# Kernel tuning notes

Hardware: AMD Instinct MI355X
Metric: run time of the kernel (lower is better)

Reference implementation:

```python
import jax, jax.numpy as jnp
import numpy as np


def _patch_indices():
    # 36 positions (6x6 grid), each gathering a 3x3 window of 6-channel squares
    # from the flattened 385-vector: index = x*48 + y*6 + c
    idx = []
    for i in range(36):
        x, y = i // 6, i % 6
        rows = []
        for ox in range(3):
            for oy in range(3):
                base = (x + ox) * 48 + (y + oy) * 6
                rows.extend(range(base, base + 6))
        idx.append(rows)
    return jnp.asarray(np.array(idx, dtype=np.int32))  # [36, 54]


_IDX = _patch_indices()


def _crelu(v):
    return jnp.clip(v, -1.0, 1.0)


def setup_inputs() -> dict:
    key = jax.random.key(0)
    ks = jax.random.split(key, 13)
    B = 131072
    inp = jax.random.normal(ks[0], (B, 385), dtype=jnp.float32)
    s = 0.2  # small init scale
    # sight stack: 54 -> 8 -> 8 -> 1  (stored as [in, out])
    W1 = jax.random.normal(ks[1], (54, 8), jnp.float32) * s
    b1 = jax.random.normal(ks[2], (8,), jnp.float32) * s
    W2 = jax.random.normal(ks[3], (8, 8), jnp.float32) * s
    b2 = jax.random.normal(ks[4], (8,), jnp.float32) * s
    W3 = jax.random.normal(ks[5], (8, 1), jnp.float32) * s
    b3 = jax.random.normal(ks[6], (1,), jnp.float32) * s
    # evaluation stack: 37 -> 16 -> 16 -> 1
    E1 = jax.random.normal(ks[7], (37, 16), jnp.float32) * s
    c1 = jax.random.normal(ks[8], (16,), jnp.float32) * s
    E2 = jax.random.normal(ks[9], (16, 16), jnp.float32) * s
    c2 = jax.random.normal(ks[10], (16,), jnp.float32) * s
    E3 = jax.random.normal(ks[11], (16, 1), jnp.float32) * s
    c3 = jax.random.normal(ks[12], (1,), jnp.float32) * s
    return {"inp": inp, "W1": W1, "b1": b1, "W2": W2, "b2": b2,
            "W3": W3, "b3": b3, "E1": E1, "c1": c1, "E2": E2, "c2": c2,
            "E3": E3, "c3": c3}


def reference(inp, W1, b1, W2, b2, W3, b3, E1, c1, E2, c2, E3, c3):
    # inp: [B, 385]
    patches = inp[:, _IDX]                       # [B, 36, 54] windowed gather
    h = _crelu(jnp.einsum('bpf,fo->bpo', patches, W1) + b1)   # [B, 36, 8]
    h = _crelu(jnp.einsum('bpf,fo->bpo', h, W2) + b2)         # [B, 36, 8]
    v = _crelu(jnp.einsum('bpf,fo->bpo', h, W3) + b3)[..., 0]  # [B, 36]
    vision = jnp.concatenate([v, inp[:, 384:385]], axis=1)    # [B, 37]
    g = _crelu(vision @ E1 + c1)                 # [B, 16]
    g = _crelu(g @ E2 + c2)                      # [B, 16]
    out = _crelu(g @ E3 + c3)                    # [B, 1]
    return out
```

## Files before the change

kernel.cpp:

```cpp
#include <hip/hip_runtime.h>

typedef __attribute__((ext_vector_type(8))) short short8;
typedef __attribute__((ext_vector_type(4))) float float4v;

__device__ __forceinline__ float crelu(float v) {
    return fminf(1.0f, fmaxf(-1.0f, v));
}
__device__ __forceinline__ uint f2bf_u(float v) {
    uint u = __float_as_uint(v);
    u += 0x7fffu + ((u >> 16) & 1u);
    return u >> 16;
}
__device__ __forceinline__ ushort f2bf(float v) { return (ushort)f2bf_u(v); }
__device__ __forceinline__ float bf2f_lo(uint u) { return __uint_as_float(u << 16); }
__device__ __forceinline__ float bf2f_hi(uint u) { return __uint_as_float(u & 0xffff0000u); }
__device__ __forceinline__ uint cvt_pk_bf16(float a, float b) {
    uint r;
    asm("v_cvt_pk_bf16_f32 %0, %1, %2" : "=v"(r) : "v"(a), "v"(b));
    return r;
}

#define ROW 385
#define BT  16

#define SLAB_BYTES 6656
#define E1T_OFF 960
#define E2T_OFF 3776
#define E1T_LD  44

__global__ __launch_bounds__(256, 6)
void lila_wave(const float* __restrict__ inp,
               const float* __restrict__ W1, const float* __restrict__ b1,
               const float* __restrict__ W2, const float* __restrict__ b2,
               const float* __restrict__ W3, const float* __restrict__ b3,
               const float* __restrict__ E1, const float* __restrict__ c1,
               const float* __restrict__ E2, const float* __restrict__ c2,
               const float* __restrict__ E3, const float* __restrict__ c3,
               float* __restrict__ out)
{
    __shared__ __align__(16) char slab_all[4 * SLAB_BYTES];

    const int tid  = threadIdx.x;
    const int lane = tid & 63;
    const int wv   = tid >> 6;
    const int quad = lane >> 4;
    const int nn   = lane & 15;
    const int m0   = quad * 8;

    char*   slab  = slab_all + wv * SLAB_BYTES;
    ushort* board = (ushort*)slab;
    ushort* hbuf  = (ushort*)(slab + 4352);
    float*  vis   = (float*)slab;
    float*  g1    = (float*)(slab + 640);
    float*  e1t   = (float*)(slab + E1T_OFF);
    ushort* e2t   = (ushort*)(slab + E2T_OFF);

    const long long b0w = (long long)blockIdx.x * BT + wv * 4;

    short8 bfr[3];
    #pragma unroll
    for (int rr = 0; rr < 3; ++rr) {
        #pragma unroll
        for (int j = 0; j < 8; ++j) {
            int k = m0 + j, oy = k >> 3, c = k & 7;
            float w = (oy < 3 && c < 6 && nn < 8)
                    ? W1[(rr * 18 + oy * 6 + c) * 8 + nn] : 0.0f;
            bfr[rr][j] = (short)f2bf(w);
        }
    }
    const float bias1 = (nn < 8) ? b1[nn] : 0.0f;

    short8 w2fh, w2fl;
    {
        const int colq = nn - quad * 8;
        #pragma unroll
        for (int j = 0; j < 8; ++j) {
            float w = (quad < 2 && colq >= 0 && colq < 8) ? W2[j * 8 + colq] : 0.0f;
            uint hb2 = f2bf_u(w);
            float wr = w - __uint_as_float(hb2 << 16);
            w2fh[j] = (short)hb2;
            w2fl[j] = (short)f2bf(wr);
        }
    }
    const float b2v = b2[nn & 7];
    const float w3v = W3[nn & 7];
    const float b3v = b3[0];
    const float c1v = c1[nn];
    const float c2v = c2[nn];
    const float e3v = E3[nn];

    const int r   = lane >> 4;
    const int c16 = lane & 15;
    const float* gr = inp + (b0w + r) * ROW;

    if (c16 < 4) {
        uint4 z = {0u, 0u, 0u, 0u};
        *(uint4*)(board + r * 544 + 512 + c16 * 8) = z;
    }
    #pragma unroll
    for (int u = 0; u < 4; ++u) {
        int cell = c16 + 16 * u;
        int g = cell * 6;
        float4 q0 = *(const float4*)(gr + g);
        float2 q1 = *(const float2*)(gr + g + 4);
        uint4 pk;
        pk.x = cvt_pk_bf16(q0.x, q0.y);
        pk.y = cvt_pk_bf16(q0.z, q0.w);
        pk.z = cvt_pk_bf16(q1.x, q1.y);
        pk.w = 0u;
        *(uint4*)(board + r * 544 + cell * 8) = pk;
    }
    const float cen = gr[384];

    asm volatile("" ::: "memory");

    {
        const int lb0 = nn >> 2, y0 = nn & 3;
        const ushort* base = board + lb0 * 544 + 8 * y0 + m0;
        union { uint4 u; short8 s; } rw[3];
        rw[0].u = *(const uint4*)(base);
        rw[1].u = *(const uint4*)(base + 64);
        #pragma unroll
        for (int x = 0; x < 6; ++x) {
            rw[(x + 2) % 3].u = *(const uint4*)(base + (x + 2) * 64);
            float4v acc = { bias1, bias1, bias1, bias1 };
            acc = __builtin_amdgcn_mfma_f32_16x16x32_bf16(rw[x % 3].s,       bfr[0], acc, 0, 0, 0);
            acc = __builtin_amdgcn_mfma_f32_16x16x32_bf16(rw[(x + 1) % 3].s, bfr[1], acc, 0, 0, 0);
            acc = __builtin_amdgcn_mfma_f32_16x16x32_bf16(rw[(x + 2) % 3].s, bfr[2], acc, 0, 0, 0);
            if (nn < 8) {
                uint w01 = cvt_pk_bf16(crelu(acc[0]), crelu(acc[1]));
                uint w23 = cvt_pk_bf16(crelu(acc[2]), crelu(acc[3]));
                ushort* hb = hbuf + (quad * 36 + x * 6) * 8 + nn;
                hb[0]  = (ushort)w01;
                hb[8]  = (ushort)(w01 >> 16);
                hb[16] = (ushort)w23;
                hb[24] = (ushort)(w23 >> 16);
            }
        }
    }
    {
        const int lb1 = (nn >> 1) & 3, y1 = 4 + (nn & 1);
        const ushort* base = board + lb1 * 544 + 8 * y1 + m0;
        union { uint4 u; short8 s; } rw[3];
        rw[0].u = *(const uint4*)(base);
        rw[1].u = *(const uint4*)(base + 64);
        #pragma unroll
        for (int x = 0; x < 6; ++x) {
            rw[(x + 2) % 3].u = *(const uint4*)(base + (x + 2) * 64);
            float4v acc = { bias1, bias1, bias1, bias1 };
            acc = __builtin_amdgcn_mfma_f32_16x16x32_bf16(rw[x % 3].s,       bfr[0], acc, 0, 0, 0);
            acc = __builtin_amdgcn_mfma_f32_16x16x32_bf16(rw[(x + 1) % 3].s, bfr[1], acc, 0, 0, 0);
            acc = __builtin_amdgcn_mfma_f32_16x16x32_bf16(rw[(x + 2) % 3].s, bfr[2], acc, 0, 0, 0);
            if (quad < 2 && nn < 8) {
                uint w01 = cvt_pk_bf16(crelu(acc[0]), crelu(acc[1]));
                uint w23 = cvt_pk_bf16(crelu(acc[2]), crelu(acc[3]));
                ushort* hb = hbuf + ((2 * quad) * 36 + x * 6 + 4) * 8 + nn;
                hb[0]   = (ushort)w01;
                hb[8]   = (ushort)(w01 >> 16);
                hb[288] = (ushort)w23;
                hb[296] = (ushort)(w23 >> 16);
            }
        }
    }

    asm volatile("" ::: "memory");

    float e1g[10];
    #pragma unroll
    for (int k = 0; k < 9; ++k) e1g[k] = E1[lane + 64 * k];
    if (lane < 16) e1g[9] = E1[lane + 576];
    float e2g[4];
    #pragma unroll
    for (int k = 0; k < 4; ++k) e2g[k] = E2[lane + 64 * k];

    {
        #pragma unroll
        for (int t = 0; t < 5; ++t) {
            union { uint4 u; short8 s; } av;
            av.u.x = 0u; av.u.y = 0u; av.u.z = 0u; av.u.w = 0u;
            int tsk = t * 16 + nn + (quad ? 80 : 0);
            if (quad < 2 && (t < 4 || quad == 0))
                av.u = *(const uint4*)(hbuf + tsk * 8);
            float4v acc = { b2v, b2v, b2v, b2v };
            acc = __builtin_amdgcn_mfma_f32_16x16x32_bf16(av.s, w2fh, acc, 0, 0, 0);
            acc = __builtin_amdgcn_mfma_f32_16x16x32_bf16(av.s, w2fl, acc, 0, 0, 0);
            float vsum[4];
            #pragma unroll
            for (int i = 0; i < 4; ++i) {
                float vv = crelu(acc[i]) * w3v;
                vv += __shfl_xor(vv, 1);
                vv += __shfl_xor(vv, 2);
                vv += __shfl_xor(vv, 4);
                vsum[i] = vv;
            }
            const bool isA = (nn == 0);
            if ((nn & 7) == 0 && (isA || t < 4)) {
                int task = (isA ? 0 : 80) + t * 16 + quad * 4;
                uint lb = (uint)task / 36u;
                uint p  = (uint)task - 36u * lb;
                float4 o4;
                o4.x = crelu(vsum[0] + b3v);
                o4.y = crelu(vsum[1] + b3v);
                o4.z = crelu(vsum[2] + b3v);
                o4.w = crelu(vsum[3] + b3v);
                *(float4*)(vis + lb * 40 + p) = o4;
            }
        }
    }

    #pragma unroll
    for (int k = 0; k < 9; ++k) e1t[nn * E1T_LD + r + 4 * k] = e1g[k];
    if (lane < 16) e1t[nn * E1T_LD + 36] = e1g[9];
    #pragma unroll
    for (int k = 0; k < 4; ++k) e2t[nn * 16 + r + 4 * k] = f2bf(e2g[k]);

    asm volatile("" ::: "memory");

    {
        const int o = nn;
        float a = c1v;
        #pragma unroll
        for (int fi = 0; fi < 9; ++fi) {
            float4 vv = *(const float4*)(vis + r * 40 + fi * 4);
            float4 ev = *(const float4*)(e1t + o * E1T_LD + fi * 4);
            a = fmaf(vv.x, ev.x, a);
            a = fmaf(vv.y, ev.y, a);
            a = fmaf(vv.z, ev.z, a);
            a = fmaf(vv.w, ev.w, a);
        }
        a = fmaf(cen, e1t[o * E1T_LD + 36], a);
        g1[r * 20 + o] = crelu(a);

        asm volatile("" ::: "memory");

        uint4 e2a = *(const uint4*)(e2t + o * 16);
        uint4 e2b = *(const uint4*)(e2t + o * 16 + 8);
        float a2 = c2v;
        #pragma unroll
        for (int fi = 0; fi < 4; ++fi) {
            float4 gv = *(const float4*)(g1 + r * 20 + fi * 4);
            uint w01 = (fi < 2) ? (fi == 0 ? e2a.x : e2a.z) : (fi == 2 ? e2b.x : e2b.z);
            uint w23 = (fi < 2) ? (fi == 0 ? e2a.y : e2a.w) : (fi == 2 ? e2b.y : e2b.w);
            a2 = fmaf(gv.x, bf2f_lo(w01), a2);
            a2 = fmaf(gv.y, bf2f_hi(w01), a2);
            a2 = fmaf(gv.z, bf2f_lo(w23), a2);
            a2 = fmaf(gv.w, bf2f_hi(w23), a2);
        }
        float tv = crelu(a2) * e3v;
        tv += __shfl_xor(tv, 1);
        tv += __shfl_xor(tv, 2);
        tv += __shfl_xor(tv, 4);
        tv += __shfl_xor(tv, 8);
        if (o == 0) out[b0w + r] = crelu(tv + c3[0]);
    }
}

extern "C" void kernel_launch(void* const* d_in, const int* in_sizes, int n_in,
                              void* d_out, int out_size, void* d_ws, size_t ws_size,
                              hipStream_t stream)
{
    const float* inp = (const float*)d_in[0];
    const float* W1  = (const float*)d_in[1];
    const float* b1  = (const float*)d_in[2];
    const float* W2  = (const float*)d_in[3];
    const float* b2  = (const float*)d_in[4];
    const float* W3  = (const float*)d_in[5];
    const float* b3  = (const float*)d_in[6];
    const float* E1  = (const float*)d_in[7];
    const float* c1  = (const float*)d_in[8];
    const float* E2  = (const float*)d_in[9];
    const float* c2  = (const float*)d_in[10];
    const float* E3  = (const float*)d_in[11];
    const float* c3  = (const float*)d_in[12];
    float* out = (float*)d_out;

    int B = in_sizes[0] / ROW;
    int grid = B / BT;
    lila_wave<<<grid, 256, 0, stream>>>(inp, W1, b1, W2, b2, W3, b3,
                                        E1, c1, E2, c2, E3, c3, out);
}
```

Measured before the change: 295.8 us.

## Make kernel persistent over 8 row groups with register prefetch and shared weight tables

Each wave now processes 8 groups of 4 rows in a loop instead of one, prefetching the next group's input into registers while computing the current one. The weight loads and the E1/E2 transposed tables are moved out of the per-group path: the tables are built once per block by wave 0 in shared memory and published with a barrier. The grid shrinks by a factor of 8 and launch bounds drop to 4 blocks per SIMD, trading occupancy and extra registers for amortized setup and overlap of global loads with compute.

```diff
diff --git a/kernel.cpp b/kernel.cpp
--- a/kernel.cpp
+++ b/kernel.cpp
@@ -22,13 +22,13 @@
 
 #define ROW 385
 #define BT  16
-
-#define SLAB_BYTES 6656
-#define E1T_OFF 960
-#define E2T_OFF 3776
-#define E1T_LD  44
-
-__global__ __launch_bounds__(256, 6)
+#define NG  8
+
+#define TAB_BYTES  3392
+#define SLAB_BYTES 7616
+#define E1T_LD     44
+
+__global__ __launch_bounds__(256, 4)
 void lila_wave(const float* __restrict__ inp,
                const float* __restrict__ W1, const float* __restrict__ b1,
                const float* __restrict__ W2, const float* __restrict__ b2,
@@ -38,7 +38,7 @@
                const float* __restrict__ E3, const float* __restrict__ c3,
                float* __restrict__ out)
 {
-    __shared__ __align__(16) char slab_all[4 * SLAB_BYTES];
+    __shared__ __align__(16) char slab_all[TAB_BYTES + 4 * SLAB_BYTES];
 
     const int tid  = threadIdx.x;
     const int lane = tid & 63;
@@ -46,16 +46,31 @@
     const int quad = lane >> 4;
     const int nn   = lane & 15;
     const int m0   = quad * 8;
-
-    char*   slab  = slab_all + wv * SLAB_BYTES;
+    const int r    = lane >> 4;
+    const int c16  = lane & 15;
+
+    char*   slab  = slab_all + TAB_BYTES + wv * SLAB_BYTES;
     ushort* board = (ushort*)slab;
     ushort* hbuf  = (ushort*)(slab + 4352);
-    float*  vis   = (float*)slab;
-    float*  g1    = (float*)(slab + 640);
-    float*  e1t   = (float*)(slab + E1T_OFF);
-    ushort* e2t   = (ushort*)(slab + E2T_OFF);
-
-    const long long b0w = (long long)blockIdx.x * BT + wv * 4;
+    float*  vis   = (float*)(slab + 6656);
+    float*  g1    = (float*)(slab + 7296);
+    float*  e1t   = (float*)slab_all;
+    ushort* e2t   = (ushort*)(slab_all + 2816);
+
+    const long long s0 = (long long)blockIdx.x * (BT * NG) + (long long)wv * (4 * NG);
+    const float* grp = inp + s0 * ROW;
+
+    float4 p4[4]; float2 p2[4]; float cen_c;
+    {
+        const float* gr = grp + r * ROW;
+        #pragma unroll
+        for (int u = 0; u < 4; ++u) {
+            int g6 = (c16 + 16 * u) * 6;
+            p4[u] = *(const float4*)(gr + g6);
+            p2[u] = *(const float2*)(gr + g6 + 4);
+        }
+        cen_c = gr[384];
+    }
 
     short8 bfr[3];
     #pragma unroll
@@ -89,169 +104,195 @@
     const float c2v = c2[nn];
     const float e3v = E3[nn];
 
-    const int r   = lane >> 4;
-    const int c16 = lane & 15;
-    const float* gr = inp + (b0w + r) * ROW;
+    if (wv == 0) {
+        float e1g[10];
+        #pragma unroll
+        for (int k = 0; k < 9; ++k) e1g[k] = E1[lane + 64 * k];
+        if (lane < 16) e1g[9] = E1[lane + 576];
+        float e2g[4];
+        #pragma unroll
+        for (int k = 0; k < 4; ++k) e2g[k] = E2[lane + 64 * k];
+        #pragma unroll
+        for (int k = 0; k < 9; ++k) e1t[nn * E1T_LD + r + 4 * k] = e1g[k];
+        if (lane < 16) e1t[nn * E1T_LD + 36] = e1g[9];
+        #pragma unroll
+        for (int k = 0; k < 4; ++k) e2t[nn * 16 + r + 4 * k] = f2bf(e2g[k]);
+    }
 
     if (c16 < 4) {
         uint4 z = {0u, 0u, 0u, 0u};
         *(uint4*)(board + r * 544 + 512 + c16 * 8) = z;
     }
+
     #pragma unroll
     for (int u = 0; u < 4; ++u) {
         int cell = c16 + 16 * u;
-        int g = cell * 6;
-        float4 q0 = *(const float4*)(gr + g);
-        float2 q1 = *(const float2*)(gr + g + 4);
         uint4 pk;
-        pk.x = cvt_pk_bf16(q0.x, q0.y);
-        pk.y = cvt_pk_bf16(q0.z, q0.w);
-        pk.z = cvt_pk_bf16(q1.x, q1.y);
+        pk.x = cvt_pk_bf16(p4[u].x, p4[u].y);
+        pk.y = cvt_pk_bf16(p4[u].z, p4[u].w);
+        pk.z = cvt_pk_bf16(p2[u].x, p2[u].y);
         pk.w = 0u;
         *(uint4*)(board + r * 544 + cell * 8) = pk;
     }
-    const float cen = gr[384];
-
-    asm volatile("" ::: "memory");
-
-    {
-        const int lb0 = nn >> 2, y0 = nn & 3;
-        const ushort* base = board + lb0 * 544 + 8 * y0 + m0;
-        union { uint4 u; short8 s; } rw[3];
-        rw[0].u = *(const uint4*)(base);
-        rw[1].u = *(const uint4*)(base + 64);
-        #pragma unroll
-        for (int x = 0; x < 6; ++x) {
-            rw[(x + 2) % 3].u = *(const uint4*)(base + (x + 2) * 64);
-            float4v acc = { bias1, bias1, bias1, bias1 };
-            acc = __builtin_amdgcn_mfma_f32_16x16x32_bf16(rw[x % 3].s,       bfr[0], acc, 0, 0, 0);
-            acc = __builtin_amdgcn_mfma_f32_16x16x32_bf16(rw[(x + 1) % 3].s, bfr[1], acc, 0, 0, 0);
-            acc = __builtin_amdgcn_mfma_f32_16x16x32_bf16(rw[(x + 2) % 3].s, bfr[2], acc, 0, 0, 0);
-            if (nn < 8) {
-                uint w01 = cvt_pk_bf16(crelu(acc[0]), crelu(acc[1]));
-                uint w23 = cvt_pk_bf16(crelu(acc[2]), crelu(acc[3]));
-                ushort* hb = hbuf + (quad * 36 + x * 6) * 8 + nn;
-                hb[0]  = (ushort)w01;
-                hb[8]  = (ushort)(w01 >> 16);
-                hb[16] = (ushort)w23;
-                hb[24] = (ushort)(w23 >> 16);
-            }
-        }
-    }
-    {
-        const int lb1 = (nn >> 1) & 3, y1 = 4 + (nn & 1);
-        const ushort* base = board + lb1 * 544 + 8 * y1 + m0;
-        union { uint4 u; short8 s; } rw[3];
-        rw[0].u = *(const uint4*)(base);
-        rw[1].u = *(const uint4*)(base + 64);
-        #pragma unroll
-        for (int x = 0; x < 6; ++x) {
-            rw[(x + 2) % 3].u = *(const uint4*)(base + (x + 2) * 64);
-            float4v acc = { bias1, bias1, bias1, bias1 };
-            acc = __builtin_amdgcn_mfma_f32_16x16x32_bf16(rw[x % 3].s,       bfr[0], acc, 0, 0, 0);
-            acc = __builtin_amdgcn_mfma_f32_16x16x32_bf16(rw[(x + 1) % 3].s, bfr[1], acc, 0, 0, 0);
-            acc = __builtin_amdgcn_mfma_f32_16x16x32_bf16(rw[(x + 2) % 3].s, bfr[2], acc, 0, 0, 0);
-            if (quad < 2 && nn < 8) {
-                uint w01 = cvt_pk_bf16(crelu(acc[0]), crelu(acc[1]));
-                uint w23 = cvt_pk_bf16(crelu(acc[2]), crelu(acc[3]));
-                ushort* hb = hbuf + ((2 * quad) * 36 + x * 6 + 4) * 8 + nn;
-                hb[0]   = (ushort)w01;
-                hb[8]   = (ushort)(w01 >> 16);
-                hb[288] = (ushort)w23;
-                hb[296] = (ushort)(w23 >> 16);
-            }
-        }
-    }
-
-    asm volatile("" ::: "memory");
-
-    float e1g[10];
-    #pragma unroll
-    for (int k = 0; k < 9; ++k) e1g[k] = E1[lane + 64 * k];
-    if (lane < 16) e1g[9] = E1[lane + 576];
-    float e2g[4];
-    #pragma unroll
-    for (int k = 0; k < 4; ++k) e2g[k] = E2[lane + 64 * k];
-
-    {
-        #pragma unroll
-        for (int t = 0; t < 5; ++t) {
-            union { uint4 u; short8 s; } av;
-            av.u.x = 0u; av.u.y = 0u; av.u.z = 0u; av.u.w = 0u;
-            int tsk = t * 16 + nn + (quad ? 80 : 0);
-            if (quad < 2 && (t < 4 || quad == 0))
-                av.u = *(const uint4*)(hbuf + tsk * 8);
-            float4v acc = { b2v, b2v, b2v, b2v };
-            acc = __builtin_amdgcn_mfma_f32_16x16x32_bf16(av.s, w2fh, acc, 0, 0, 0);
-            acc = __builtin_amdgcn_mfma_f32_16x16x32_bf16(av.s, w2fl, acc, 0, 0, 0);
-            float vsum[4];
-            #pragma unroll
-            for (int i = 0; i < 4; ++i) {
-                float vv = crelu(acc[i]) * w3v;
-                vv += __shfl_xor(vv, 1);
-                vv += __shfl_xor(vv, 2);
-                vv += __shfl_xor(vv, 4);
-                vsum[i] = vv;
-            }
-            const bool isA = (nn == 0);
-            if ((nn & 7) == 0 && (isA || t < 4)) {
-                int task = (isA ? 0 : 80) + t * 16 + quad * 4;
-                uint lb = (uint)task / 36u;
-                uint p  = (uint)task - 36u * lb;
-                float4 o4;
-                o4.x = crelu(vsum[0] + b3v);
-                o4.y = crelu(vsum[1] + b3v);
-                o4.z = crelu(vsum[2] + b3v);
-                o4.w = crelu(vsum[3] + b3v);
-                *(float4*)(vis + lb * 40 + p) = o4;
-            }
-        }
-    }
-
-    #pragma unroll
-    for (int k = 0; k < 9; ++k) e1t[nn * E1T_LD + r + 4 * k] = e1g[k];
-    if (lane < 16) e1t[nn * E1T_LD + 36] = e1g[9];
-    #pragma unroll
-    for (int k = 0; k < 4; ++k) e2t[nn * 16 + r + 4 * k] = f2bf(e2g[k]);
-
-    asm volatile("" ::: "memory");
-
-    {
-        const int o = nn;
-        float a = c1v;
-        #pragma unroll
-        for (int fi = 0; fi < 9; ++fi) {
-            float4 vv = *(const float4*)(vis + r * 40 + fi * 4);
-            float4 ev = *(const float4*)(e1t + o * E1T_LD + fi * 4);
-            a = fmaf(vv.x, ev.x, a);
-            a = fmaf(vv.y, ev.y, a);
-            a = fmaf(vv.z, ev.z, a);
-            a = fmaf(vv.w, ev.w, a);
-        }
-        a = fmaf(cen, e1t[o * E1T_LD + 36], a);
-        g1[r * 20 + o] = crelu(a);
+
+    __syncthreads();
+
+    #pragma unroll 1
+    for (int gi = 0; gi < NG; ++gi) {
+        float4 p4n[4]; float2 p2n[4]; float cen_n = 0.0f;
+        grp += 4 * ROW;
+        if (gi + 1 < NG) {
+            const float* gr = grp + r * ROW;
+            #pragma unroll
+            for (int u = 0; u < 4; ++u) {
+                int g6 = (c16 + 16 * u) * 6;
+                p4n[u] = *(const float4*)(gr + g6);
+                p2n[u] = *(const float2*)(gr + g6 + 4);
+            }
+            cen_n = gr[384];
+        }
+
+        {
+            const int lb0 = nn >> 2, y0 = nn & 3;
+            const ushort* base = board + lb0 * 544 + 8 * y0 + m0;
+            union { uint4 u; short8 s; } rw[3];
+            rw[0].u = *(const uint4*)(base);
+            rw[1].u = *(const uint4*)(base + 64);
+            #pragma unroll
+            for (int x = 0; x < 6; ++x) {
+                rw[(x + 2) % 3].u = *(const uint4*)(base + (x + 2) * 64);
+                float4v acc = { bias1, bias1, bias1, bias1 };
+                acc = __builtin_amdgcn_mfma_f32_16x16x32_bf16(rw[x % 3].s,       bfr[0], acc, 0, 0, 0);
+                acc = __builtin_amdgcn_mfma_f32_16x16x32_bf16(rw[(x + 1) % 3].s, bfr[1], acc, 0, 0, 0);
+                acc = __builtin_amdgcn_mfma_f32_16x16x32_bf16(rw[(x + 2) % 3].s, bfr[2], acc, 0, 0, 0);
+                if (nn < 8) {
+                    uint w01 = cvt_pk_bf16(crelu(acc[0]), crelu(acc[1]));
+                    uint w23 = cvt_pk_bf16(crelu(acc[2]), crelu(acc[3]));
+                    ushort* hb = hbuf + (quad * 36 + x * 6) * 8 + nn;
+                    hb[0]  = (ushort)w01;
+                    hb[8]  = (ushort)(w01 >> 16);
+                    hb[16] = (ushort)w23;
+                    hb[24] = (ushort)(w23 >> 16);
+                }
+            }
+        }
+        {
+            const int lb1 = (nn >> 1) & 3, y1 = 4 + (nn & 1);
+            const ushort* base = board + lb1 * 544 + 8 * y1 + m0;
+            union { uint4 u; short8 s; } rw[3];
+            rw[0].u = *(const uint4*)(base);
+            rw[1].u = *(const uint4*)(base + 64);
+            #pragma unroll
+            for (int x = 0; x < 6; ++x) {
+                rw[(x + 2) % 3].u = *(const uint4*)(base + (x + 2) * 64);
+                float4v acc = { bias1, bias1, bias1, bias1 };
+                acc = __builtin_amdgcn_mfma_f32_16x16x32_bf16(rw[x % 3].s,       bfr[0], acc, 0, 0, 0);
+                acc = __builtin_amdgcn_mfma_f32_16x16x32_bf16(rw[(x + 1) % 3].s, bfr[1], acc, 0, 0, 0);
+                acc = __builtin_amdgcn_mfma_f32_16x16x32_bf16(rw[(x + 2) % 3].s, bfr[2], acc, 0, 0, 0);
+                if (quad < 2 && nn < 8) {
+                    uint w01 = cvt_pk_bf16(crelu(acc[0]), crelu(acc[1]));
+                    uint w23 = cvt_pk_bf16(crelu(acc[2]), crelu(acc[3]));
+                    ushort* hb = hbuf + ((2 * quad) * 36 + x * 6 + 4) * 8 + nn;
+                    hb[0]   = (ushort)w01;
+                    hb[8]   = (ushort)(w01 >> 16);
+                    hb[288] = (ushort)w23;
+                    hb[296] = (ushort)(w23 >> 16);
+                }
+            }
+        }
 
         asm volatile("" ::: "memory");
 
-        uint4 e2a = *(const uint4*)(e2t + o * 16);
-        uint4 e2b = *(const uint4*)(e2t + o * 16 + 8);
-        float a2 = c2v;
-        #pragma unroll
-        for (int fi = 0; fi < 4; ++fi) {
-            float4 gv = *(const float4*)(g1 + r * 20 + fi * 4);
-            uint w01 = (fi < 2) ? (fi == 0 ? e2a.x : e2a.z) : (fi == 2 ? e2b.x : e2b.z);
-            uint w23 = (fi < 2) ? (fi == 0 ? e2a.y : e2a.w) : (fi == 2 ? e2b.y : e2b.w);
-            a2 = fmaf(gv.x, bf2f_lo(w01), a2);
-            a2 = fmaf(gv.y, bf2f_hi(w01), a2);
-            a2 = fmaf(gv.z, bf2f_lo(w23), a2);
-            a2 = fmaf(gv.w, bf2f_hi(w23), a2);
-        }
-        float tv = crelu(a2) * e3v;
-        tv += __shfl_xor(tv, 1);
-        tv += __shfl_xor(tv, 2);
-        tv += __shfl_xor(tv, 4);
-        tv += __shfl_xor(tv, 8);
-        if (o == 0) out[b0w + r] = crelu(tv + c3[0]);
+        if (gi + 1 < NG) {
+            #pragma unroll
+            for (int u = 0; u < 4; ++u) {
+                int cell = c16 + 16 * u;
+                uint4 pk;
+                pk.x = cvt_pk_bf16(p4n[u].x, p4n[u].y);
+                pk.y = cvt_pk_bf16(p4n[u].z, p4n[u].w);
+                pk.z = cvt_pk_bf16(p2n[u].x, p2n[u].y);
+                pk.w = 0u;
+                *(uint4*)(board + r * 544 + cell * 8) = pk;
+            }
+        }
+
+        {
+            #pragma unroll
+            for (int t = 0; t < 5; ++t) {
+                union { uint4 u; short8 s; } av;
+                av.u.x = 0u; av.u.y = 0u; av.u.z = 0u; av.u.w = 0u;
+                int tsk = t * 16 + nn + (quad ? 80 : 0);
+                if (quad < 2 && (t < 4 || quad == 0))
+                    av.u = *(const uint4*)(hbuf + tsk * 8);
+                float4v acc = { b2v, b2v, b2v, b2v };
+                acc = __builtin_amdgcn_mfma_f32_16x16x32_bf16(av.s, w2fh, acc, 0, 0, 0);
+                acc = __builtin_amdgcn_mfma_f32_16x16x32_bf16(av.s, w2fl, acc, 0, 0, 0);
+                float vsum[4];
+                #pragma unroll
+                for (int i = 0; i < 4; ++i) {
+                    float vv = crelu(acc[i]) * w3v;
+                    vv += __shfl_xor(vv, 1);
+                    vv += __shfl_xor(vv, 2);
+                    vv += __shfl_xor(vv, 4);
+                    vsum[i] = vv;
+                }
+                const bool isA = (nn == 0);
+                if ((nn & 7) == 0 && (isA || t < 4)) {
+                    int task = (isA ? 0 : 80) + t * 16 + quad * 4;
+                    uint lb = (uint)task / 36u;
+                    uint p  = (uint)task - 36u * lb;
+                    float4 o4;
+                    o4.x = crelu(vsum[0] + b3v);
+                    o4.y = crelu(vsum[1] + b3v);
+                    o4.z = crelu(vsum[2] + b3v);
+                    o4.w = crelu(vsum[3] + b3v);
+                    *(float4*)(vis + lb * 40 + p) = o4;
+                }
+            }
+        }
+
+        asm volatile("" ::: "memory");
+
+        {
+            const int o = nn;
+            float a = c1v;
+            #pragma unroll
+            for (int fi = 0; fi < 9; ++fi) {
+                float4 vv = *(const float4*)(vis + r * 40 + fi * 4);
+                float4 ev = *(const float4*)(e1t + o * E1T_LD + fi * 4);
+                a = fmaf(vv.x, ev.x, a);
+                a = fmaf(vv.y, ev.y, a);
+                a = fmaf(vv.z, ev.z, a);
+                a = fmaf(vv.w, ev.w, a);
+            }
+            a = fmaf(cen_c, e1t[o * E1T_LD + 36], a);
+            g1[r * 20 + o] = crelu(a);
+
+            asm volatile("" ::: "memory");
+
+            uint4 e2a = *(const uint4*)(e2t + o * 16);
+            uint4 e2b = *(const uint4*)(e2t + o * 16 + 8);
+            float a2 = c2v;
+            #pragma unroll
+            for (int fi = 0; fi < 4; ++fi) {
+                float4 gv = *(const float4*)(g1 + r * 20 + fi * 4);
+                uint w01 = (fi < 2) ? (fi == 0 ? e2a.x : e2a.z) : (fi == 2 ? e2b.x : e2b.z);
+                uint w23 = (fi < 2) ? (fi == 0 ? e2a.y : e2a.w) : (fi == 2 ? e2b.y : e2b.w);
+                a2 = fmaf(gv.x, bf2f_lo(w01), a2);
+                a2 = fmaf(gv.y, bf2f_hi(w01), a2);
+                a2 = fmaf(gv.z, bf2f_lo(w23), a2);
+                a2 = fmaf(gv.w, bf2f_hi(w23), a2);
+            }
+            float tv = crelu(a2) * e3v;
+            tv += __shfl_xor(tv, 1);
+            tv += __shfl_xor(tv, 2);
+            tv += __shfl_xor(tv, 4);
+            tv += __shfl_xor(tv, 8);
+            if (o == 0) out[s0 + gi * 4 + r] = crelu(tv + c3[0]);
+        }
+
+        cen_c = cen_n;
+        asm volatile("" ::: "memory");
     }
 }
 
@@ -275,7 +316,7 @@
     float* out = (float*)d_out;
 
     int B = in_sizes[0] / ROW;
-    int grid = B / BT;
+    int grid = B / (BT * NG);
     lila_wave<<<grid, 256, 0, stream>>>(inp, W1, b1, W2, b2, W3, b3,
                                         E1, c1, E2, c2, E3, c3, out);
 }
```

Result: slower. 311.8 us (+5.4%).
